# Kernel optimization log

Hardware: AMD Instinct MI355X
Metric: run time of the kernel (lower is better)

The kernel has to match this reference:

```python
import math
import jax, jax.numpy as jnp
import numpy as np

B, S, IN_DIM, D_MODEL, L, T_Y = 16, 512, 64, 64, 32, 256
T_X = T_Y + L - 1
RIDGE = 0.01
THRESH = 0.005


def _pos_encoding(seq_len, d):
    pos = jnp.arange(seq_len, dtype=jnp.float32)[:, None]
    div = jnp.exp(jnp.arange(0, d, 2, dtype=jnp.float32) * (-(math.log(10000.0) / d)))
    ang = pos * div  # [S, d/2]
    pe = jnp.zeros((seq_len, d), dtype=jnp.float32)
    pe = pe.at[:, 0::2].set(jnp.sin(ang)).at[:, 1::2].set(jnp.cos(ang))
    return pe


def _layernorm(h, gamma, beta, eps=1e-5):
    mu = jnp.mean(h, axis=-1, keepdims=True)
    var = jnp.mean((h - mu) ** 2, axis=-1, keepdims=True)
    return (h - mu) * jax.lax.rsqrt(var + eps) * gamma + beta


def setup_inputs() -> dict:
    key = jax.random.key(0)
    ks = jax.random.split(key, 8)
    return {
        "fps": jax.random.normal(ks[0], (B, S, IN_DIM), dtype=jnp.float32),
        "x": jax.random.normal(ks[1], (B, S, T_X), dtype=jnp.float32),
        "y": jax.random.normal(ks[2], (B, S, T_Y), dtype=jnp.float32),
        "sample_steps": jax.random.randint(ks[3], (5,), 10, S),
        "W1": jax.random.normal(ks[4], (IN_DIM, 256), dtype=jnp.float32) / math.sqrt(IN_DIM),
        "b1": jnp.zeros((256,), dtype=jnp.float32),
        "gamma": jnp.ones((256,), dtype=jnp.float32),
        "beta": jnp.zeros((256,), dtype=jnp.float32),
        "W2": jax.random.normal(ks[5], (256, D_MODEL), dtype=jnp.float32) / math.sqrt(256.0),
        "b2": jnp.zeros((D_MODEL,), dtype=jnp.float32),
        "Wq": jax.random.normal(ks[6], (D_MODEL, D_MODEL), dtype=jnp.float32) / math.sqrt(D_MODEL),
        "bq": jnp.zeros((D_MODEL,), dtype=jnp.float32),
        "Wk": jax.random.normal(ks[7], (D_MODEL, D_MODEL), dtype=jnp.float32) / math.sqrt(D_MODEL),
        "bk": jnp.zeros((D_MODEL,), dtype=jnp.float32),
    }


def reference(fps, x, y, sample_steps, W1, b1, gamma, beta, W2, b2, Wq, bq, Wk, bk):
    batch, seq_len, _ = fps.shape
    d = Wq.shape[0]
    t_y = y.shape[-1]
    filt = x.shape[-1] - t_y + 1  # L

    # encoder: Linear -> LayerNorm -> Tanh -> Linear -> Tanh
    h = _layernorm(fps @ W1 + b1, gamma, beta)
    e_orig = jnp.tanh(jnp.tanh(h) @ W2 + b2)  # [B,S,d]
    e = e_orig + 0.05 * _pos_encoding(seq_len, d)[None]

    q = e @ Wq + bq
    k = e @ Wk + bk
    scores = jnp.einsum('bsd,btd->bst', q, k) / math.sqrt(d)
    causal = jnp.triu(jnp.ones((seq_len, seq_len), dtype=bool), 1)
    scores = jnp.where(causal[None], -1e9, scores)
    alpha = jax.nn.softmax(scores * 2.0, axis=-1)  # [B,S,S]

    # sliding windows: X[b,s] = unfold(x[b,s], L, 1)[:T_y] -> [T_y, L]
    win = jnp.arange(t_y)[:, None] + jnp.arange(filt)[None, :]
    X = x[:, :, win]  # [B,S,T_y,L]

    # per-source gram / cross contributions
    G = jnp.einsum('bstl,bstm->bslm', X, X)  # [B,S,L,L]
    C = jnp.einsum('bstl,bst->bsl', X, y)    # [B,S,L]

    w = alpha[:, sample_steps, :]            # [B,T,S]
    wm = jnp.where(w > THRESH, w, 0.0)

    gram = jnp.einsum('bts,bslm->btlm', wm, G) + RIDGE * jnp.eye(filt, dtype=x.dtype)
    cross = jnp.einsum('bts,bsl->btl', wm, C)
    wt_hat = jnp.linalg.solve(gram, cross[..., None])[..., 0]  # [B,T,L]

    Xt = X[:, sample_steps]  # [B,T,T_y,L]
    yt = y[:, sample_steps]  # [B,T,T_y]
    pred = jnp.einsum('btkl,btl->btk', Xt, wt_hat)
    loss_bt = jnp.mean((yt - pred) ** 2, axis=-1)  # [B,T]

    valid = jnp.any(wm > 0.0, axis=-1)  # [B,T]
    total = jnp.sum(jnp.where(valid, loss_bt, 0.0))
    n = jnp.maximum(jnp.sum(valid.astype(jnp.int32)), 1)
    loss = total / n
    return loss, alpha, e_orig
```

## Files before the change

### kernel.cpp

```cpp
#include <hip/hip_runtime.h>
#include <hip/hip_bf16.h>
#include <math.h>

#define BB 16
#define SS 512
#define INDIM 64
#define DMODEL 64
#define HID 256
#define FILT 32
#define TYY 256
#define TXX 287
#define NT 5
#define RIDGEF 0.01f
#define THRESHF 0.005f

__global__ __launch_bounds__(256) void k_mlp(
    const float* __restrict__ fps, const float* __restrict__ W1, const float* __restrict__ b1,
    const float* __restrict__ gamma, const float* __restrict__ beta,
    const float* __restrict__ W2, const float* __restrict__ b2,
    const float* __restrict__ Wq, const float* __restrict__ bq,
    const float* __restrict__ Wk, const float* __restrict__ bk,
    float* __restrict__ e_out, float* __restrict__ q_out, float* __restrict__ kT_out)
{
    const int row0 = blockIdx.x << 3;
    const int tid = threadIdx.x;
    const int wid = tid >> 6, lane = tid & 63;

    __shared__ float fr[8][INDIM];
    __shared__ float th4[8][HID];
    __shared__ float ee4[4][DMODEL];
    __shared__ float part4[4][4][DMODEL];
    __shared__ float partk4[4][4][DMODEL];
    __shared__ float wred[4][8][2];

    { int r = tid >> 6, i = tid & 63;
      fr[r][i]     = fps[(row0 + r) * INDIM + i];
      fr[r + 4][i] = fps[(row0 + r + 4) * INDIM + i]; }
    __syncthreads();

    float h[8];
    float b1v = b1[tid];
    #pragma unroll
    for (int r = 0; r < 8; ++r) h[r] = b1v;
    for (int i = 0; i < INDIM; ++i) {
        float w = W1[i * HID + tid];
        #pragma unroll
        for (int r = 0; r < 8; ++r) h[r] = fmaf(fr[r][i], w, h[r]);
    }

    float s1[8], s2[8];
    #pragma unroll
    for (int r = 0; r < 8; ++r) { s1[r] = h[r]; s2[r] = h[r] * h[r]; }
    #pragma unroll
    for (int off = 1; off < 64; off <<= 1) {
        #pragma unroll
        for (int r = 0; r < 8; ++r) {
            s1[r] += __shfl_xor(s1[r], off);
            s2[r] += __shfl_xor(s2[r], off);
        }
    }
    if (lane == 0) {
        #pragma unroll
        for (int r = 0; r < 8; ++r) { wred[wid][r][0] = s1[r]; wred[wid][r][1] = s2[r]; }
    }
    __syncthreads();
    float gm = gamma[tid], bt = beta[tid];
    #pragma unroll
    for (int r = 0; r < 8; ++r) {
        float t1 = wred[0][r][0] + wred[1][r][0] + wred[2][r][0] + wred[3][r][0];
        float t2 = wred[0][r][1] + wred[1][r][1] + wred[2][r][1] + wred[3][r][1];
        float mu = t1 * (1.0f / HID);
        float var = t2 * (1.0f / HID) - mu * mu;
        float hn = (h[r] - mu) * rsqrtf(var + 1e-5f) * gm + bt;
        th4[r][tid] = tanhf(hn);
    }
    __syncthreads();

    #pragma unroll
    for (int half = 0; half < 2; ++half) {
        const int rbase = half * 4;
        { int p = tid >> 6, j = tid & 63;
          float acc[4] = {0.f, 0.f, 0.f, 0.f};
          for (int i = p * 64; i < p * 64 + 64; ++i) {
              float w = W2[i * DMODEL + j];
              #pragma unroll
              for (int r = 0; r < 4; ++r) acc[r] = fmaf(th4[rbase + r][i], w, acc[r]);
          }
          #pragma unroll
          for (int r = 0; r < 4; ++r) part4[p][r][j] = acc[r];
        }
        __syncthreads();
        { int r = tid >> 6, j = tid & 63;
          float e = part4[0][r][j] + part4[1][r][j] + part4[2][r][j] + part4[3][r][j] + b2[j];
          float eo = tanhf(e);
          int row = row0 + rbase + r;
          int s = row & (SS - 1);
          e_out[(size_t)row * DMODEL + j] = eo;
          float div = expf(-(float)(j & ~1) * 0.14391156831212787f);
          float ang = (float)s * div;
          float pe = (j & 1) ? cosf(ang) : sinf(ang);
          ee4[r][j] = eo + 0.05f * pe;
        }
        __syncthreads();
        { int p = tid >> 6, j = tid & 63;
          float aq[4] = {0.f,0.f,0.f,0.f}, ak[4] = {0.f,0.f,0.f,0.f};
          for (int i = p * 16; i < p * 16 + 16; ++i) {
              float wqv = Wq[i * DMODEL + j];
              float wkv = Wk[i * DMODEL + j];
              #pragma unroll
              for (int r = 0; r < 4; ++r) {
                  aq[r] = fmaf(ee4[r][i], wqv, aq[r]);
                  ak[r] = fmaf(ee4[r][i], wkv, ak[r]);
              }
          }
          #pragma unroll
          for (int r = 0; r < 4; ++r) { part4[p][r][j] = aq[r]; partk4[p][r][j] = ak[r]; }
        }
        __syncthreads();
        { int r = tid >> 6, j = tid & 63;
          float qv = part4[0][r][j] + part4[1][r][j] + part4[2][r][j] + part4[3][r][j] + bq[j];
          float kv = partk4[0][r][j] + partk4[1][r][j] + partk4[2][r][j] + partk4[3][r][j] + bk[j];
          int row = row0 + rbase + r;
          int b = row >> 9, s = row & (SS - 1);
          q_out[(size_t)row * DMODEL + j] = qv;
          kT_out[(size_t)(b * DMODEL + j) * SS + s] = kv;
        }
        __syncthreads();
    }
}

__global__ __launch_bounds__(256) void k_attn(
    const float* __restrict__ q, const float* __restrict__ kT,
    float* __restrict__ alpha)
{
    const int blk = blockIdx.x;
    const int b = blk >> 7;
    const int t0 = (blk & 127) << 2;
    const int t3 = t0 + 3;
    const int tid = threadIdx.x;
    const int wave = tid >> 6, lane = tid & 63;

    __shared__ float qt[4 * DMODEL];
    __shared__ float redm[4][4];

    qt[tid] = q[(size_t)(b * SS + t0 + (tid >> 6)) * DMODEL + (tid & 63)];
    __syncthreads();

    const float* kTb = kT + (size_t)b * DMODEL * SS;
    const int s0 = tid, s1 = tid + 256;
    float a0[4] = {0,0,0,0}, a1[4] = {0,0,0,0};
    if (s1 <= t3) {
        for (int d = 0; d < DMODEL; ++d) {
            float k0 = kTb[d * SS + s0];
            float k1 = kTb[d * SS + s1];
            #pragma unroll
            for (int r = 0; r < 4; ++r) {
                float qv = qt[r * DMODEL + d];
                a0[r] = fmaf(qv, k0, a0[r]);
                a1[r] = fmaf(qv, k1, a1[r]);
            }
        }
    } else if (s0 <= t3) {
        for (int d = 0; d < DMODEL; ++d) {
            float k0 = kTb[d * SS + s0];
            #pragma unroll
            for (int r = 0; r < 4; ++r) a0[r] = fmaf(qt[r * DMODEL + d], k0, a0[r]);
        }
    }
    float lg0[4], lg1[4];
    #pragma unroll
    for (int r = 0; r < 4; ++r) {
        int tr = t0 + r;
        lg0[r] = (s0 <= tr) ? 0.25f * a0[r] : -INFINITY;
        lg1[r] = (s1 <= tr) ? 0.25f * a1[r] : -INFINITY;
    }
    float mr[4];
    #pragma unroll
    for (int r = 0; r < 4; ++r) {
        float m = fmaxf(lg0[r], lg1[r]);
        #pragma unroll
        for (int off = 32; off > 0; off >>= 1) m = fmaxf(m, __shfl_xor(m, off));
        if (lane == 0) redm[r][wave] = m;
    }
    __syncthreads();
    #pragma unroll
    for (int r = 0; r < 4; ++r)
        mr[r] = fmaxf(fmaxf(redm[r][0], redm[r][1]), fmaxf(redm[r][2], redm[r][3]));
    __syncthreads();
    float ex0[4], ex1[4], sr[4];
    #pragma unroll
    for (int r = 0; r < 4; ++r) {
        ex0[r] = expf(lg0[r] - mr[r]);
        ex1[r] = expf(lg1[r] - mr[r]);
        float sm = ex0[r] + ex1[r];
        #pragma unroll
        for (int off = 32; off > 0; off >>= 1) sm += __shfl_xor(sm, off);
        if (lane == 0) redm[r][wave] = sm;
    }
    __syncthreads();
    #pragma unroll
    for (int r = 0; r < 4; ++r)
        sr[r] = redm[r][0] + redm[r][1] + redm[r][2] + redm[r][3];
    #pragma unroll
    for (int r = 0; r < 4; ++r) {
        float inv = 1.0f / sr[r];
        size_t base = (size_t)(b * SS + t0 + r) * SS;
        alpha[base + s0] = ex0[r] * inv;
        alpha[base + s1] = ex1[r] * inv;
    }
}

__global__ __launch_bounds__(256) void k_gpart(
    const float* __restrict__ x, const float* __restrict__ y,
    const int* __restrict__ steps, const float* __restrict__ alpha,
    float* __restrict__ part, int C, int CS)
{
    const int b = blockIdx.x / C;
    const int chunk = blockIdx.x % C;
    const int tid = threadIdx.x;
    const int lane = tid & 63, wid = tid >> 6;

    __shared__ __align__(16) float xs[288];
    __shared__ __align__(16) float ys[256];
    __shared__ float Gs[1056];
    __shared__ float crossL[32];
    __shared__ float wv[NT * 64];
    __shared__ int sl[64];
    __shared__ int nselS;
    __shared__ int stS[NT];
    __shared__ float redA[4][33];
    __shared__ float redB[4][33];

    if (tid < NT) stS[tid] = steps[tid];
    if (tid < 32) Gs[tid * 33 + 32] = 0.f;
    __syncthreads();

    for (int idx = tid; idx < NT * CS; idx += 256) {
        int t = idx / CS, si = idx % CS;
        float a = alpha[(size_t)(b * SS + stS[t]) * SS + chunk * CS + si];
        wv[t * 64 + si] = (a > THRESHF) ? a : 0.f;
    }
    __syncthreads();
    if (tid == 0) {
        int c = 0;
        for (int si = 0; si < CS; ++si) {
            float m = wv[si] + wv[64 + si] + wv[128 + si] + wv[192 + si] + wv[256 + si];
            if (m > 0.f) sl[c++] = si;
        }
        nselS = c;
    }
    __syncthreads();
    const int nsel = nselS;

    float acc[NT][5];
    #pragma unroll
    for (int t = 0; t < NT; ++t) {
        #pragma unroll
        for (int r = 0; r < 5; ++r) acc[t][r] = 0.f;
    }

    float rx0 = 0.f, rx1 = 0.f, ry = 0.f;
    if (nsel > 0) {
        int sg = chunk * CS + sl[0];
        const float* xr = x + (size_t)(b * SS + sg) * TXX;
        const float* yr = y + (size_t)(b * SS + sg) * TYY;
        rx0 = xr[tid];
        if (tid < 31) rx1 = xr[256 + tid];
        ry = yr[tid];
    }

    for (int i = 0; i < nsel; ++i) {
        xs[tid] = rx0;
        if (tid < 31) xs[256 + tid] = rx1;
        ys[tid] = ry;
        const int sl_cur = sl[i];
        __syncthreads();

        if (i + 1 < nsel) {
            int sg = chunk * CS + sl[i + 1];
            const float* xr = x + (size_t)(b * SS + sg) * TXX;
            const float* yr = y + (size_t)(b * SS + sg) * TYY;
            rx0 = xr[tid];
            if (tid < 31) rx1 = xr[256 + tid];
            ry = yr[tid];
        }

        { int l = tid & 31, p = tid >> 5;
          const float4* xk4 = (const float4*)(xs + (p << 5));
          const float4* yk4 = (const float4*)(ys + (p << 5));
          float c = 0.f, a = 0.f;
          #pragma unroll
          for (int j = 0; j < 8; ++j) {
              float4 xk = xk4[j];
              float4 yk = yk4[j];
              int kb = (p << 5) + (j << 2);
              float x0 = xs[kb + l],     x1 = xs[kb + 1 + l];
              float x2 = xs[kb + 2 + l], x3 = xs[kb + 3 + l];
              c = fmaf(x0, yk.x, c); a = fmaf(xk.x, x0, a);
              c = fmaf(x1, yk.y, c); a = fmaf(xk.y, x1, a);
              c = fmaf(x2, yk.z, c); a = fmaf(xk.z, x2, a);
              c = fmaf(x3, yk.w, c); a = fmaf(xk.w, x3, a);
          }
          c += __shfl_xor(c, 32);
          a += __shfl_xor(a, 32);
          if (lane < 32) { redA[wid][l] = c; redB[wid][l] = a; }
        }
        __syncthreads();

        if (tid < 32)
            crossL[tid] = redA[0][tid] + redA[1][tid] + redA[2][tid] + redA[3][tid];

        { int jj = lane & 31;
          #pragma unroll
          for (int pass = 0; pass < 4; ++pass) {
              int dd = 2 * (wid + 4 * pass) + (lane >> 5);
              float g0 = redB[0][dd] + redB[1][dd] + redB[2][dd] + redB[3][dd];
              float dlt = 0.f;
              if (jj > 0 && jj + dd < 32)
                  dlt = xs[jj + 255] * xs[jj + 255 + dd]
                      - xs[jj - 1] * xs[jj - 1 + dd];
              #pragma unroll
              for (int off = 1; off < 32; off <<= 1) {
                  float tsh = __shfl_up(dlt, off, 32);
                  if (jj >= off) dlt += tsh;
              }
              if (jj + dd < 32) {
                  float gval = g0 + dlt;
                  Gs[jj * 33 + jj + dd] = gval;
                  Gs[(jj + dd) * 33 + jj] = gval;
              }
          }
        }
        __syncthreads();

        { float g0 = Gs[tid], g1 = Gs[tid + 256], g2 = Gs[tid + 512], g3 = Gs[tid + 768];
          float g4 = (tid < 32) ? Gs[1024 + tid]
                   : ((tid < 64) ? crossL[tid - 32] : 0.f);
          #pragma unroll
          for (int t = 0; t < NT; ++t) {
              float w = wv[t * 64 + sl_cur];
              if (w > 0.f) {
                  acc[t][0] = fmaf(w, g0, acc[t][0]);
                  acc[t][1] = fmaf(w, g1, acc[t][1]);
                  acc[t][2] = fmaf(w, g2, acc[t][2]);
                  acc[t][3] = fmaf(w, g3, acc[t][3]);
                  acc[t][4] = fmaf(w, g4, acc[t][4]);
              }
          }
        }
    }

    #pragma unroll
    for (int t = 0; t < NT; ++t) {
        size_t base = (size_t)((b * NT + t) * C + chunk) * 1088;
        #pragma unroll
        for (int r = 0; r < 4; ++r) part[base + tid + 256 * r] = acc[t][r];
        if (tid < 64) part[base + 1024 + tid] = acc[t][4];
    }
}

__global__ __launch_bounds__(256) void k_reduce(
    const float* __restrict__ part, float* __restrict__ gram, int C)
{
    const int g = blockIdx.x / 5;
    const int seg = blockIdx.x % 5;
    const int tid = threadIdx.x;
    int idx = seg * 256 + tid;
    if (idx >= 1088) return;

    const float* pp = part + (size_t)g * C * 1088 + idx;
    float s0 = 0.f, s1 = 0.f, s2 = 0.f, s3 = 0.f;
    int ch = 0;
    for (; ch + 4 <= C; ch += 4) {
        s0 += pp[(size_t)(ch + 0) * 1088];
        s1 += pp[(size_t)(ch + 1) * 1088];
        s2 += pp[(size_t)(ch + 2) * 1088];
        s3 += pp[(size_t)(ch + 3) * 1088];
    }
    for (; ch < C; ++ch) s0 += pp[(size_t)ch * 1088];
    gram[(size_t)g * 1088 + idx] = (s0 + s1) + (s2 + s3);
}

__global__ __launch_bounds__(256) void k_solve2(
    const float* __restrict__ x, const float* __restrict__ y,
    const int* __restrict__ steps, const float* __restrict__ alpha,
    const float* __restrict__ gram,
    float* __restrict__ lossbt, int* __restrict__ valid)
{
    const int g = blockIdx.x;
    const int b = g / NT, t = g % NT;
    const int tid = threadIdx.x;

    __shared__ float Af[1056];
    __shared__ float zs[FILT];
    __shared__ float wt[FILT];
    __shared__ float xsr[TXX + 1];
    __shared__ float red[256];
    __shared__ int step_s;
    __shared__ int anyv;

    if (tid == 0) { step_s = steps[t]; anyv = 0; }
    __syncthreads();

    const float* row = gram + (size_t)g * 1088;
    Af[tid] = row[tid];
    Af[tid + 256] = row[tid + 256];
    Af[tid + 512] = row[tid + 512];
    Af[tid + 768] = row[tid + 768];
    if (tid < 32) Af[1024 + tid] = row[1024 + tid];
    else if (tid < 64) zs[tid - 32] = row[1024 + tid];

    { const float* arow = alpha + (size_t)(b * SS + step_s) * SS;
      if (arow[tid] > THRESHF || arow[tid + 256] > THRESHF) anyv = 1; }
    __syncthreads();
    if (tid < 32) Af[tid * 33 + tid] += RIDGEF;
    __syncthreads();

    if (tid < 32) {
        float a[32];
        #pragma unroll
        for (int j = 0; j < 32; ++j) a[j] = Af[tid * 33 + j];
        #pragma unroll
        for (int k = 0; k < 32; ++k) {
            float akk = __shfl(a[k], k);
            float dk = sqrtf(akk);
            float ck = a[k] / dk;
            if (tid >= k) a[k] = ck;
            #pragma unroll
            for (int m = k + 1; m < 32; ++m) {
                float cm = __shfl(ck, m);
                if (tid >= m) a[m] = fmaf(-ck, cm, a[m]);
            }
        }
        #pragma unroll
        for (int j = 0; j < 32; ++j)
            if (j <= tid) Af[tid * 33 + j] = a[j];

        float zl = zs[tid];
        #pragma unroll
        for (int k = 0; k < 32; ++k) {
            float akk = __shfl(a[k], k);
            float zk = __shfl(zl, k) / akk;
            if (tid == k) zl = zk;
            else if (tid > k) zl = fmaf(-a[k], zk, zl);
        }
        #pragma unroll
        for (int k = 31; k >= 0; --k) {
            float akk = __shfl(a[k], k);
            float wk = __shfl(zl, k) / akk;
            if (tid == k) zl = wk;
            else if (tid < k) zl = fmaf(-Af[k * 33 + tid], wk, zl);
        }
        wt[tid] = zl;
    }
    __syncthreads();

    const int sstep = step_s;
    const float* xrow = x + (size_t)(b * SS + sstep) * TXX;
    for (int i = tid; i < TXX; i += 256) xsr[i] = xrow[i];
    __syncthreads();
    float pk = 0.f;
    #pragma unroll
    for (int l = 0; l < FILT; ++l) pk = fmaf(xsr[tid + l], wt[l], pk);
    float d = y[(size_t)(b * SS + sstep) * TYY + tid] - pk;
    red[tid] = d * d;
    __syncthreads();
    for (int off = 128; off > 0; off >>= 1) {
        if (tid < off) red[tid] += red[tid + off];
        __syncthreads();
    }
    if (tid == 0) {
        lossbt[g] = red[0] * (1.0f / TYY);
        valid[g] = anyv;
    }
}

__global__ __launch_bounds__(128) void k_final(
    const float* __restrict__ lossbt, const int* __restrict__ valid,
    float* __restrict__ out0)
{
    __shared__ float rs[128];
    __shared__ int rc[128];
    int tid = threadIdx.x;
    float v = 0.f; int c = 0;
    if (tid < BB * NT && valid[tid]) { v = lossbt[tid]; c = 1; }
    rs[tid] = v; rc[tid] = c;
    __syncthreads();
    for (int off = 64; off > 0; off >>= 1) {
        if (tid < off) { rs[tid] += rs[tid + off]; rc[tid] += rc[tid + off]; }
        __syncthreads();
    }
    if (tid == 0) {
        int n = rc[0] > 0 ? rc[0] : 1;
        out0[0] = rs[0] / (float)n;
    }
}

extern "C" void kernel_launch(void* const* d_in, const int* in_sizes, int n_in,
                              void* d_out, int out_size, void* d_ws, size_t ws_size,
                              hipStream_t stream)
{
    const float* fps  = (const float*)d_in[0];
    const float* x    = (const float*)d_in[1];
    const float* y    = (const float*)d_in[2];
    const int* steps  = (const int*)d_in[3];
    const float* W1   = (const float*)d_in[4];
    const float* b1   = (const float*)d_in[5];
    const float* gamma= (const float*)d_in[6];
    const float* beta = (const float*)d_in[7];
    const float* W2   = (const float*)d_in[8];
    const float* b2   = (const float*)d_in[9];
    const float* Wq   = (const float*)d_in[10];
    const float* bq   = (const float*)d_in[11];
    const float* Wk   = (const float*)d_in[12];
    const float* bk   = (const float*)d_in[13];

    float* out   = (float*)d_out;
    float* alpha = out + 1;
    float* e_out = out + 1 + (size_t)BB * SS * SS;

    float* lossbt = (float*)d_ws;
    int*   valid  = (int*)(lossbt + 128);
    float* gram   = (float*)d_ws + 256;
    float* shreg  = gram + (size_t)BB * NT * 1088;
    float* q      = shreg;
    float* kT     = q + (size_t)BB * SS * DMODEL;
    float* part   = shreg;

    size_t head_f = 256 + (size_t)BB * NT * 1088;
    size_t avail_f = (ws_size / 4 > head_f) ? (ws_size / 4 - head_f) : 0;
    int C = 64;
    while (C > 8 && (size_t)(BB * NT) * C * 1088 > avail_f) C >>= 1;
    int CS = SS / C;

    hipLaunchKernelGGL(k_mlp, dim3(BB * SS / 8), dim3(256), 0, stream,
                       fps, W1, b1, gamma, beta, W2, b2, Wq, bq, Wk, bk,
                       e_out, q, kT);
    hipLaunchKernelGGL(k_attn, dim3(BB * (SS / 4)), dim3(256), 0, stream,
                       q, kT, alpha);
    hipLaunchKernelGGL(k_gpart, dim3(BB * C), dim3(256), 0, stream,
                       x, y, steps, alpha, part, C, CS);
    hipLaunchKernelGGL(k_reduce, dim3(BB * NT * 5), dim3(256), 0, stream,
                       part, gram, C);
    hipLaunchKernelGGL(k_solve2, dim3(BB * NT), dim3(256), 0, stream,
                       x, y, steps, alpha, gram, lossbt, valid);
    hipLaunchKernelGGL(k_final, dim3(1), dim3(128), 0, stream, lossbt, valid, out);
}
```

Measured before the change: 208.6 us.

## Replace partial-sum reduce and final kernels with atomics and last-block finish

k_gpart now accumulates its per-chunk gram/cross contributions straight into a gram buffer with atomicAdd, and only for steps whose chunk weight is nonzero. The gram buffer and counters are zeroed inside k_mlp, so the partial buffer and the k_reduce launch are no longer needed. The final loss mean moves into k_solve2 using a last-block-done counter pattern, which removes the k_final launch. The serial selection loop is also replaced with a wave ballot/popcount compaction. The cost is atomic contention on gram (up to 64 chunks per batch) and results whose float summation order varies from run to run.

```diff
diff --git a/kernel.cpp b/kernel.cpp
--- a/kernel.cpp
+++ b/kernel.cpp
@@ -13,6 +13,8 @@
 #define NT 5
 #define RIDGEF 0.01f
 #define THRESHF 0.005f
+#define GRAMN 1088
+#define GRAMTOT (BB * NT * GRAMN)
 
 __global__ __launch_bounds__(256) void k_mlp(
     const float* __restrict__ fps, const float* __restrict__ W1, const float* __restrict__ b1,
@@ -20,11 +22,18 @@
     const float* __restrict__ W2, const float* __restrict__ b2,
     const float* __restrict__ Wq, const float* __restrict__ bq,
     const float* __restrict__ Wk, const float* __restrict__ bk,
-    float* __restrict__ e_out, float* __restrict__ q_out, float* __restrict__ kT_out)
+    float* __restrict__ e_out, float* __restrict__ q_out, float* __restrict__ kT_out,
+    float* __restrict__ gram, int* __restrict__ ctrs)
 {
     const int row0 = blockIdx.x << 3;
     const int tid = threadIdx.x;
     const int wid = tid >> 6, lane = tid & 63;
+
+    if (blockIdx.x < GRAMTOT / 256) {
+        gram[(size_t)blockIdx.x * 256 + tid] = 0.f;
+    } else if (blockIdx.x == GRAMTOT / 256 && tid < 4) {
+        ctrs[tid] = 0;
+    }
 
     __shared__ float fr[8][INDIM];
     __shared__ float th4[8][HID];
@@ -213,7 +222,7 @@
 __global__ __launch_bounds__(256) void k_gpart(
     const float* __restrict__ x, const float* __restrict__ y,
     const int* __restrict__ steps, const float* __restrict__ alpha,
-    float* __restrict__ part, int C, int CS)
+    float* __restrict__ gram, int C, int CS)
 {
     const int b = blockIdx.x / C;
     const int chunk = blockIdx.x % C;
@@ -225,6 +234,7 @@
     __shared__ float Gs[1056];
     __shared__ float crossL[32];
     __shared__ float wv[NT * 64];
+    __shared__ float wtot[NT];
     __shared__ int sl[64];
     __shared__ int nselS;
     __shared__ int stS[NT];
@@ -241,13 +251,21 @@
         wv[t * 64 + si] = (a > THRESHF) ? a : 0.f;
     }
     __syncthreads();
-    if (tid == 0) {
-        int c = 0;
-        for (int si = 0; si < CS; ++si) {
-            float m = wv[si] + wv[64 + si] + wv[128 + si] + wv[192 + si] + wv[256 + si];
-            if (m > 0.f) sl[c++] = si;
-        }
-        nselS = c;
+    if (tid < NT) {
+        float s = 0.f;
+        for (int si = 0; si < CS; ++si) s += wv[tid * 64 + si];
+        wtot[tid] = s;
+    }
+    if (wid == 0) {
+        float m = 0.f;
+        if (lane < CS)
+            m = wv[lane] + wv[64 + lane] + wv[128 + lane] + wv[192 + lane] + wv[256 + lane];
+        unsigned long long mask = __ballot(m > 0.f);
+        if (m > 0.f) {
+            int pos = __popcll(mask & ((1ull << lane) - 1ull));
+            sl[pos] = lane;
+        }
+        if (lane == 0) nselS = __popcll(mask);
     }
     __syncthreads();
     const int nsel = nselS;
@@ -352,40 +370,20 @@
 
     #pragma unroll
     for (int t = 0; t < NT; ++t) {
-        size_t base = (size_t)((b * NT + t) * C + chunk) * 1088;
-        #pragma unroll
-        for (int r = 0; r < 4; ++r) part[base + tid + 256 * r] = acc[t][r];
-        if (tid < 64) part[base + 1024 + tid] = acc[t][4];
-    }
-}
-
-__global__ __launch_bounds__(256) void k_reduce(
-    const float* __restrict__ part, float* __restrict__ gram, int C)
-{
-    const int g = blockIdx.x / 5;
-    const int seg = blockIdx.x % 5;
-    const int tid = threadIdx.x;
-    int idx = seg * 256 + tid;
-    if (idx >= 1088) return;
-
-    const float* pp = part + (size_t)g * C * 1088 + idx;
-    float s0 = 0.f, s1 = 0.f, s2 = 0.f, s3 = 0.f;
-    int ch = 0;
-    for (; ch + 4 <= C; ch += 4) {
-        s0 += pp[(size_t)(ch + 0) * 1088];
-        s1 += pp[(size_t)(ch + 1) * 1088];
-        s2 += pp[(size_t)(ch + 2) * 1088];
-        s3 += pp[(size_t)(ch + 3) * 1088];
-    }
-    for (; ch < C; ++ch) s0 += pp[(size_t)ch * 1088];
-    gram[(size_t)g * 1088 + idx] = (s0 + s1) + (s2 + s3);
+        if (wtot[t] > 0.f) {
+            float* gr = gram + (size_t)(b * NT + t) * GRAMN;
+            #pragma unroll
+            for (int r = 0; r < 4; ++r) atomicAdd(&gr[tid + 256 * r], acc[t][r]);
+            if (tid < 64) atomicAdd(&gr[1024 + tid], acc[t][4]);
+        }
+    }
 }
 
 __global__ __launch_bounds__(256) void k_solve2(
     const float* __restrict__ x, const float* __restrict__ y,
     const int* __restrict__ steps, const float* __restrict__ alpha,
     const float* __restrict__ gram,
-    float* __restrict__ lossbt, int* __restrict__ valid)
+    int* __restrict__ ctrs, float* __restrict__ out0)
 {
     const int g = blockIdx.x;
     const int b = g / NT, t = g % NT;
@@ -402,7 +400,7 @@
     if (tid == 0) { step_s = steps[t]; anyv = 0; }
     __syncthreads();
 
-    const float* row = gram + (size_t)g * 1088;
+    const float* row = gram + (size_t)g * GRAMN;
     Af[tid] = row[tid];
     Af[tid + 256] = row[tid + 256];
     Af[tid + 512] = row[tid + 512];
@@ -470,29 +468,19 @@
         __syncthreads();
     }
     if (tid == 0) {
-        lossbt[g] = red[0] * (1.0f / TYY);
-        valid[g] = anyv;
-    }
-}
-
-__global__ __launch_bounds__(128) void k_final(
-    const float* __restrict__ lossbt, const int* __restrict__ valid,
-    float* __restrict__ out0)
-{
-    __shared__ float rs[128];
-    __shared__ int rc[128];
-    int tid = threadIdx.x;
-    float v = 0.f; int c = 0;
-    if (tid < BB * NT && valid[tid]) { v = lossbt[tid]; c = 1; }
-    rs[tid] = v; rc[tid] = c;
-    __syncthreads();
-    for (int off = 64; off > 0; off >>= 1) {
-        if (tid < off) { rs[tid] += rs[tid + off]; rc[tid] += rc[tid + off]; }
-        __syncthreads();
-    }
-    if (tid == 0) {
-        int n = rc[0] > 0 ? rc[0] : 1;
-        out0[0] = rs[0] / (float)n;
+        float lossval = red[0] * (1.0f / TYY);
+        float* loss_sum = (float*)(ctrs + 2);
+        if (anyv) {
+            atomicAdd(loss_sum, lossval);
+            atomicAdd(&ctrs[1], 1);
+        }
+        __threadfence();
+        int prev = atomicAdd(&ctrs[0], 1);
+        if (prev == BB * NT - 1) {
+            float s = atomicAdd(loss_sum, 0.0f);
+            int c = atomicAdd(&ctrs[1], 0);
+            out0[0] = s / (float)(c > 0 ? c : 1);
+        }
     }
 }
 
@@ -519,30 +507,20 @@
     float* alpha = out + 1;
     float* e_out = out + 1 + (size_t)BB * SS * SS;
 
-    float* lossbt = (float*)d_ws;
-    int*   valid  = (int*)(lossbt + 128);
-    float* gram   = (float*)d_ws + 256;
-    float* shreg  = gram + (size_t)BB * NT * 1088;
-    float* q      = shreg;
-    float* kT     = q + (size_t)BB * SS * DMODEL;
-    float* part   = shreg;
-
-    size_t head_f = 256 + (size_t)BB * NT * 1088;
-    size_t avail_f = (ws_size / 4 > head_f) ? (ws_size / 4 - head_f) : 0;
-    int C = 64;
-    while (C > 8 && (size_t)(BB * NT) * C * 1088 > avail_f) C >>= 1;
-    int CS = SS / C;
+    float* gram = (float*)d_ws;
+    int*   ctrs = (int*)(gram + GRAMTOT);
+    float* q    = (float*)(ctrs + 4);
+    float* kT   = q + (size_t)BB * SS * DMODEL;
+
+    const int C = 64, CS = SS / 64;
 
     hipLaunchKernelGGL(k_mlp, dim3(BB * SS / 8), dim3(256), 0, stream,
                        fps, W1, b1, gamma, beta, W2, b2, Wq, bq, Wk, bk,
-                       e_out, q, kT);
+                       e_out, q, kT, gram, ctrs);
     hipLaunchKernelGGL(k_attn, dim3(BB * (SS / 4)), dim3(256), 0, stream,
                        q, kT, alpha);
     hipLaunchKernelGGL(k_gpart, dim3(BB * C), dim3(256), 0, stream,
-                       x, y, steps, alpha, part, C, CS);
-    hipLaunchKernelGGL(k_reduce, dim3(BB * NT * 5), dim3(256), 0, stream,
-                       part, gram, C);
+                       x, y, steps, alpha, gram, C, CS);
     hipLaunchKernelGGL(k_solve2, dim3(BB * NT), dim3(256), 0, stream,
-                       x, y, steps, alpha, gram, lossbt, valid);
-    hipLaunchKernelGGL(k_final, dim3(1), dim3(128), 0, stream, lossbt, valid, out);
+                       x, y, steps, alpha, gram, ctrs, out);
 }
```

Result: faster. 200.2 us (-4.0%).
